# Performance work log

Hardware: AMD Instinct MI355X
Metric: run time of the kernel (lower is better)

## Reference

```python
import jax, jax.numpy as jnp
import numpy as np
from jax import lax

NUM_CLASSES = 80
CONF_THRE = 0.01   # testconf in source
NMS_THRE = 0.2     # nmsthresh in source
N = 8400           # YOLOX anchors at 640x640: 80^2+40^2+20^2
IMG = 640.0


def setup_inputs() -> dict:
    key = jax.random.key(0)
    pred = jax.random.uniform(key, (N, 5 + NUM_CLASSES), dtype=jnp.float32)
    # scale cx,cy,w,h to pixel units so boxes are realistic
    pred = pred.at[:, :4].multiply(IMG)
    return {"prediction": pred}


def _pairwise_iou(boxes):
    # boxes: [N,4] in x1,y1,x2,y2
    area = (boxes[:, 2] - boxes[:, 0]) * (boxes[:, 3] - boxes[:, 1])  # [N]
    lt = jnp.maximum(boxes[:, None, :2], boxes[None, :, :2])  # [N,N,2]
    rb = jnp.minimum(boxes[:, None, 2:], boxes[None, :, 2:])  # [N,N,2]
    wh = jnp.clip(rb - lt, 0.0)
    inter = wh[..., 0] * wh[..., 1]
    return inter / (area[:, None] + area[None, :] - inter + 1e-9)


def reference(prediction):
    # ---- box corner decode (cx,cy,w,h -> x1,y1,x2,y2) ----
    cx, cy, w, h = prediction[:, 0], prediction[:, 1], prediction[:, 2], prediction[:, 3]
    boxes = jnp.stack([cx - w / 2, cy - h / 2, cx + w / 2, cy + h / 2], axis=1)

    # ---- per-class max ----
    cls_scores = prediction[:, 5:5 + NUM_CLASSES]
    class_conf = jnp.max(cls_scores, axis=1, keepdims=True)            # [N,1]
    class_pred = jnp.argmax(cls_scores, axis=1).astype(prediction.dtype)[:, None]

    obj = prediction[:, 4]
    valid = obj >= CONF_THRE                                            # conf mask

    # detections = [x1,y1,x2,y2, obj_conf, class_conf, class_pred]  -> [N,7]
    det = jnp.concatenate([boxes, obj[:, None], class_conf, class_pred], axis=1)

    # ---- class-agnostic greedy NMS on obj score (fixed-shape version) ----
    scores = jnp.where(valid, obj, -1.0)
    order = jnp.argsort(-scores)
    det_s = det[order]
    boxes_s = boxes[order]
    valid_s = valid[order]

    iou = _pairwise_iou(boxes_s)  # [N,N] ~282MB, dominant traffic
    idx = jnp.arange(N)

    def step(keep, inp):
        i, row, v = inp
        alive = keep[i] & v                      # only a kept valid box suppresses
        supp = alive & (row > NMS_THRE) & (idx > i)
        return keep & ~supp, None

    keep0 = jnp.ones((N,), dtype=bool)
    keep, _ = lax.scan(step, keep0, (idx, iou, valid_s))
    keep = keep & valid_s

    # suppressed / below-conf rows are zeroed (torch returns a ragged subset;
    # here we return the score-sorted, mask-zeroed fixed-shape equivalent)
    out = det_s * keep[:, None].astype(det_s.dtype)
    return out
```

## Files before the change

kernel.cpp:

```cpp
#include <hip/hip_runtime.h>
#include <stdint.h>

#define N_BOX 8400
#define NCLS 80
#define PSTRIDE 85
#define NW 132
#define NTILE 8778
#define ZROWI N_BOX
#define CONF_T 0.01f
#define NMS_T 0.2f

typedef unsigned long long u64;

#define OFF_DET     0
#define OFF_DIAGT   0
#define OFF_SUP1    67584
#define OFF_SUP2    135168
#define OFF_KEYS    268800
#define OFF_DETS    336000
#define OFF_BOXESS  604800
#define OFF_MASK    739200
#define OFF_KEEPW   9610656
#define OFF_VCNT    9611712

__device__ __forceinline__ unsigned fmap_desc(float f) {
    unsigned u = __float_as_uint(f);
    unsigned m = (u & 0x80000000u) ? ~u : (u | 0x80000000u);
    return ~m;
}

__device__ __forceinline__ u64 readlane64(u64 v, int lane) {
    unsigned lo = (unsigned)__builtin_amdgcn_readlane((int)(unsigned)v, lane);
    unsigned hi = (unsigned)__builtin_amdgcn_readlane((int)(unsigned)(v >> 32), lane);
    return ((u64)hi << 32) | lo;
}

__device__ __forceinline__ u64 shfl_xor64(u64 v, int m) {
    int lo = __shfl_xor((int)(unsigned)v, m);
    int hi = __shfl_xor((int)(unsigned)(v >> 32), m);
    return ((u64)(unsigned)hi << 32) | (unsigned)lo;
}

__device__ __forceinline__ u64 bittranspose64(u64 x, int lane) {
    const u64 P0 = 0x5555555555555555ull, P1 = 0x3333333333333333ull,
              P2 = 0x0F0F0F0F0F0F0F0Full, P3 = 0x00FF00FF00FF00FFull,
              P4 = 0x0000FFFF0000FFFFull, P5 = 0x00000000FFFFFFFFull;
#define TSTEP(s, p) do {                                                 \
        u64 y = shfl_xor64(x, s);                                        \
        x = (lane & (s)) ? ((x & ~(p)) | ((y & ~(p)) >> (s)))            \
                         : ((x & (p))  | ((y & (p))  << (s)));           \
    } while (0)
    TSTEP(1, P0); TSTEP(2, P1); TSTEP(4, P2);
    TSTEP(8, P3); TSTEP(16, P4); TSTEP(32, P5);
#undef TSTEP
    return x;
}

__device__ __forceinline__ u64 wmask(int w, int V) {
    int nb = V - (w << 6);
    if (nb <= 0) return 0ull;
    if (nb >= 64) return ~0ull;
    return (1ull << nb) - 1ull;
}

__global__ __launch_bounds__(256) void prep_k(const float* __restrict__ pred,
                                              float* __restrict__ det,
                                              u64* __restrict__ keys,
                                              u64* __restrict__ mask) {
    if (blockIdx.x == 0 && threadIdx.x < NW)
        mask[(size_t)ZROWI * NW + threadIdx.x] = 0ull;
    int gt = blockIdx.x * 256 + threadIdx.x;
    int i = gt >> 2, q = gt & 3;
    if (i >= N_BOX) return;
    const float* p = pred + (size_t)i * PSTRIDE;
    int cbase = q * 20;
    float best = p[5 + cbase];
    int arg = cbase;
    for (int c = 1; c < 20; ++c) {
        float v = p[5 + cbase + c];
        if (v > best) { best = v; arg = cbase + c; }
    }
    for (int d = 1; d < 4; d <<= 1) {
        float ob = __shfl_xor(best, d);
        int   oa = __shfl_xor(arg, d);
        if (ob > best || (ob == best && oa < arg)) { best = ob; arg = oa; }
    }
    if (q == 0) {
        float cx = p[0], cy = p[1], w = p[2], h = p[3], obj = p[4];
        float hw = __fmul_rn(w, 0.5f), hh = __fmul_rn(h, 0.5f);
        float x1 = __fsub_rn(cx, hw), y1 = __fsub_rn(cy, hh);
        float x2 = __fadd_rn(cx, hw), y2 = __fadd_rn(cy, hh);
        bool valid = (obj >= CONF_T);
        float score = valid ? obj : -1.0f;
        keys[i] = ((u64)fmap_desc(score) << 32) | (unsigned)i;
        float4* dr = (float4*)(det + (size_t)i * 8);
        dr[0] = make_float4(x1, y1, x2, y2);
        dr[1] = make_float4(obj, best, (float)arg, 0.0f);
    }
}

__global__ __launch_bounds__(256) void rank_k(const u64* __restrict__ keys,
                                              const float* __restrict__ det,
                                              float4* __restrict__ det_s,
                                              float4* __restrict__ boxes_s,
                                              int* __restrict__ vcount) {
    int t = threadIdx.x;
    int i = blockIdx.x * 32 + (t & 31);
    int s = t >> 5;
    u64 my = (i < N_BOX) ? keys[i] : ~0ull;
    int cnt = 0, cv = 0;
    int j0 = s * 1050, j1 = j0 + 1050;
    for (int j = j0; j < j1; j += 2) {
        ulonglong2 kk = *(const ulonglong2*)(keys + j);
        cnt += (kk.x < my) + (kk.y < my);
        cv  += ((long long)kk.x >= 0) + ((long long)kk.y >= 0);
    }
    __shared__ int sc[256], sv[256];
    sc[t] = cnt; sv[t] = cv;
    __syncthreads();
    if (t < 32) {
        int r = sc[t] + sc[t + 32] + sc[t + 64] + sc[t + 96]
              + sc[t + 128] + sc[t + 160] + sc[t + 192] + sc[t + 224];
        if (i < N_BOX) {
            const float4* dr = (const float4*)(det + (size_t)i * 8);
            float4 b0 = dr[0], b1 = dr[1];
            det_s[(size_t)r * 2]     = b0;
            det_s[(size_t)r * 2 + 1] = b1;
            boxes_s[r] = b0;
        }
        if (blockIdx.x == 0 && t == 0) {
            *vcount = sv[0] + sv[32] + sv[64] + sv[96]
                    + sv[128] + sv[160] + sv[192] + sv[224];
        }
    }
}

__global__ __launch_bounds__(64) void mask_k(const float4* __restrict__ boxes_s,
                                             u64* __restrict__ mask,
                                             u64* __restrict__ diagT,
                                             u64* __restrict__ sup1,
                                             u64* __restrict__ sup2) {
    int tt = blockIdx.x, lane = threadIdx.x;
    int rb = (int)((2.0f * NW + 1.0f
                    - sqrtf((2.0f * NW + 1.0f) * (2.0f * NW + 1.0f) - 8.0f * (float)tt)) * 0.5f);
    while (rb > 0 && rb * NW - rb * (rb - 1) / 2 > tt) rb--;
    while ((rb + 1) * NW - (rb + 1) * rb / 2 <= tt) rb++;
    int cb = rb + (tt - (rb * NW - rb * (rb - 1) / 2));

    __shared__ float4 cB[64];
    __shared__ float  cA[64];
    int c0 = cb * 64 + lane;
    float4 b = (c0 < N_BOX) ? boxes_s[c0] : make_float4(0.f, 0.f, 0.f, 0.f);
    cB[lane] = b;
    cA[lane] = __fmul_rn(__fsub_rn(b.z, b.x), __fsub_rn(b.w, b.y));
    __syncthreads();
    int r = rb * 64 + lane;
    bool inb = (r < N_BOX);
    float4 rx = boxes_s[inb ? r : (N_BOX - 1)];
    float ra = __fmul_rn(__fsub_rn(rx.z, rx.x), __fsub_rn(rx.w, rx.y));
    u64 bits = 0ull;
    int cbase = cb * 64;
    for (int j = 0; j < 64; ++j) {
        int c = cbase + j;
        if (c >= N_BOX || c <= r) continue;
        float4 cx4 = cB[j];
        float ltx = fmaxf(rx.x, cx4.x), lty = fmaxf(rx.y, cx4.y);
        float rbx = fminf(rx.z, cx4.z), rby = fminf(rx.w, cx4.w);
        float wx = fmaxf(__fsub_rn(rbx, ltx), 0.0f);
        float wy = fmaxf(__fsub_rn(rby, lty), 0.0f);
        float inter = __fmul_rn(wx, wy);
        float denom = __fadd_rn(__fsub_rn(__fadd_rn(ra, cA[j]), inter), 1e-9f);
        float iou = __fdiv_rn(inter, denom);
        if (iou > NMS_T) bits |= (1ull << j);
    }
    if (inb) mask[(size_t)r * NW + cb] = bits;
    int d = cb - rb;
    if (d <= 2) {
        u64 tb = bittranspose64(bits, lane);
        size_t idx = (size_t)cb * 64 + lane;
        if (d == 0)      diagT[idx] = tb;
        else if (d == 1) sup1[idx]  = tb;
        else             sup2[idx]  = tb;
    }
}

__global__ __launch_bounds__(64, 1) void scan_k(const u64* __restrict__ mask,
                                                const u64* __restrict__ diagT,
                                                const u64* __restrict__ sup1,
                                                const u64* __restrict__ sup2,
                                                const int* __restrict__ vcount,
                                                u64* __restrict__ keepw) {
    int lane = threadIdx.x;
    int V = *vcount;
    int tw = (lane < 4) ? (128 + lane) : 131;
    u64 Ra = 0ull, Rb = 0ull, Rc = 0ull;
    u64 A1 = 0ull, A2 = 0ull;

#define DECLS(P) u64 P##A0=0,P##A1=0,P##A2=0,P##A3=0,P##A4=0,P##A5=0,P##A6=0,P##A7=0, \
                     P##B0=0,P##B1=0,P##B2=0,P##B3=0,P##B4=0,P##B5=0,P##B6=0,P##B7=0, \
                     P##C0=0,P##C1=0,P##C2=0,P##C3=0,P##C4=0,P##C5=0,P##C6=0,P##C7=0
    DECLS(s0); DECLS(s1); DECLS(s2);
#undef DECLS
    u64 td0,t10,t20, td1,t11,t21, td2,t12,t22, td3,t13,t23, td4,t14,t24, td5,t15,t25;

#define TLOAD(TD, T1, T2, wtv) do {                                      \
        int wt_ = (wtv); wt_ = wt_ < NW ? wt_ : (NW - 1);                \
        size_t ix_ = (size_t)wt_ * 64 + lane;                            \
        TD = diagT[ix_]; T1 = sup1[ix_]; T2 = sup2[ix_];                 \
    } while (0)

#define CONSUME(P) do {                                                  \
        Ra |= ((P##A0|P##A1)|(P##A2|P##A3))|((P##A4|P##A5)|(P##A6|P##A7));\
        Rb |= ((P##B0|P##B1)|(P##B2|P##B3))|((P##B4|P##B5)|(P##B6|P##B7));\
        Rc |= ((P##C0|P##C1)|(P##C2|P##C3))|((P##C4|P##C5)|(P##C6|P##C7));\
    } while (0)

#define ISSUE(P, i) do {                                                 \
        size_t ri_ = rem_ ? (size_t)(rb_ + __builtin_ctzll(rem_))        \
                          : (size_t)ZROWI;                               \
        rem_ &= rem_ - 1;                                                \
        const u64* rp_ = mask + ri_ * NW;                                \
        ulonglong2 v_ = *(const ulonglong2*)(rp_ + 2 * lane);            \
        P##A##i = v_.x; P##B##i = v_.y; P##C##i = rp_[tw];               \
    } while (0)

#define STEP(wv, P, TDu, T1u, T2u, TDl, T1l, T2l) do {                   \
        int w_ = (wv);                                                   \
        CONSUME(P);                          \
        TLOAD(TDl, T1l, T2l, w_ + 2);               \
        u64 rw_ = (w_ < 128) ? ((w_ & 1) ? Rb : Ra) : Rc;                \
        int sl_ = (w_ < 128) ? (w_ >> 1) : (w_ - 128);                   \
        u64 cur_ = readlane64(rw_, sl_);                                 \
        cur_ |= __ballot((T1u & A1) != 0ull);                            \
        cur_ |= __ballot((T2u & A2) != 0ull);                            \
        u64 m_ = wmask(w_, V);                                           \
        u64 ns_ = (~cur_) & m_;                                          \
        u64 L_ = 0ull;                                                   \
        while (ns_) {                           \
            int b_ = __builtin_ctzll(ns_);                               \
            L_ |= 1ull << b_;                                            \
            u64 sup_ = __ballot((int)((TDu >> b_) & 1ull));              \
            ns_ &= ~sup_;                                                \
            ns_ &= ~(1ull << b_);                                        \
        }                                                                \
        if (lane == 0) keepw[w_] = L_;                                   \
        A2 = A1; A1 = L_;                                                \
        u64 rem_ = L_; int rb_ = w_ << 6;                                \
        ISSUE(P, 0); ISSUE(P, 1); ISSUE(P, 2); ISSUE(P, 3);              \
        ISSUE(P, 4); ISSUE(P, 5); ISSUE(P, 6); ISSUE(P, 7);              \
        while (rem_) {                             \
            u64 xa_ = 0, xb_ = 0, xc_ = 0;                               \
            for (int q_ = 0; q_ < 4; ++q_) {                             \
                size_t ri_ = rem_ ? (size_t)(rb_ + __builtin_ctzll(rem_))\
                                  : (size_t)ZROWI;                       \
                rem_ &= rem_ - 1;                                        \
                const u64* rp_ = mask + ri_ * NW;                        \
                ulonglong2 v_ = *(const ulonglong2*)(rp_ + 2 * lane);    \
                xa_ |= v_.x; xb_ |= v_.y; xc_ |= rp_[tw];                \
            }                                                            \
            Ra |= xa_; Rb |= xb_; Rc |= xc_;                             \
        }                                                                \
    } while (0)

    TLOAD(td0, t10, t20, 0);
    TLOAD(td1, t11, t21, 1);

    for (int c = 0; c < NW; c += 6) {
        STEP(c + 0, s0, td0, t10, t20, td2, t12, t22);
        STEP(c + 1, s1, td1, t11, t21, td3, t13, t23);
        STEP(c + 2, s2, td2, t12, t22, td4, t14, t24);
        STEP(c + 3, s0, td3, t13, t23, td5, t15, t25);
        STEP(c + 4, s1, td4, t14, t24, td0, t10, t20);
        STEP(c + 5, s2, td5, t15, t25, td1, t11, t21);
    }
#undef STEP
#undef ISSUE
#undef CONSUME
#undef TLOAD
}

__global__ __launch_bounds__(256) void out_k(const float* __restrict__ det_s,
                                             const u64* __restrict__ keepw,
                                             float* __restrict__ out) {
    int e = blockIdx.x * 256 + threadIdx.x;
    if (e >= N_BOX * 7) return;
    int r = e / 7, c = e - r * 7;
    bool k = (keepw[r >> 6] >> (r & 63)) & 1ull;
    out[e] = k ? det_s[r * 8 + c] : 0.0f;
}

extern "C" void kernel_launch(void* const* d_in, const int* in_sizes, int n_in,
                              void* d_out, int out_size, void* d_ws, size_t ws_size,
                              hipStream_t stream) {
    const float* pred = (const float*)d_in[0];
    char* ws = (char*)d_ws;
    float*  det     = (float*) (ws + OFF_DET);
    u64*    diagT   = (u64*)   (ws + OFF_DIAGT);
    u64*    sup1    = (u64*)   (ws + OFF_SUP1);
    u64*    sup2    = (u64*)   (ws + OFF_SUP2);
    u64*    keys    = (u64*)   (ws + OFF_KEYS);
    float*  det_s   = (float*) (ws + OFF_DETS);
    float4* boxes_s = (float4*)(ws + OFF_BOXESS);
    u64*    mask    = (u64*)   (ws + OFF_MASK);
    u64*    keepw   = (u64*)   (ws + OFF_KEEPW);
    int*    vcount  = (int*)   (ws + OFF_VCNT);

    prep_k<<<132, 256, 0, stream>>>(pred, det, keys, mask);
    rank_k<<<264, 256, 0, stream>>>(keys, det, (float4*)det_s, boxes_s, vcount);
    mask_k<<<NTILE, 64, 0, stream>>>(boxes_s, mask, diagT, sup1, sup2);
    scan_k<<<1, 64, 0, stream>>>(mask, diagT, sup1, sup2, vcount, keepw);
    out_k <<<(N_BOX * 7 + 255) / 256, 256, 0, stream>>>(det_s, keepw, (float*)d_out);
}
```

Baseline: 156.3 us.

## Split NMS scan into decision and row-OR waves synchronized via LDS barriers

```diff
diff --git a/kernel.cpp b/kernel.cpp
--- a/kernel.cpp
+++ b/kernel.cpp
@@ -16,6 +16,7 @@
 #define OFF_DIAGT   0
 #define OFF_SUP1    67584
 #define OFF_SUP2    135168
+#define OFF_SUP3    202752
 #define OFF_KEYS    268800
 #define OFF_DETS    336000
 #define OFF_BOXESS  604800
@@ -61,6 +62,12 @@
     if (nb <= 0) return 0ull;
     if (nb >= 64) return ~0ull;
     return (1ull << nb) - 1ull;
+}
+
+__device__ __forceinline__ void step_barrier() {
+    asm volatile("s_waitcnt lgkmcnt(0)" ::: "memory");
+    __builtin_amdgcn_s_barrier();
+    asm volatile("" ::: "memory");
 }
 
 __global__ __launch_bounds__(256) void prep_k(const float* __restrict__ pred,
@@ -139,7 +146,8 @@
                                              u64* __restrict__ mask,
                                              u64* __restrict__ diagT,
                                              u64* __restrict__ sup1,
-                                             u64* __restrict__ sup2) {
+                                             u64* __restrict__ sup2,
+                                             u64* __restrict__ sup3) {
     int tt = blockIdx.x, lane = threadIdx.x;
     int rb = (int)((2.0f * NW + 1.0f
                     - sqrtf((2.0f * NW + 1.0f) * (2.0f * NW + 1.0f) - 8.0f * (float)tt)) * 0.5f);
@@ -175,108 +183,133 @@
     }
     if (inb) mask[(size_t)r * NW + cb] = bits;
     int d = cb - rb;
-    if (d <= 2) {
+    if (d <= 3) {
         u64 tb = bittranspose64(bits, lane);
         size_t idx = (size_t)cb * 64 + lane;
         if (d == 0)      diagT[idx] = tb;
         else if (d == 1) sup1[idx]  = tb;
-        else             sup2[idx]  = tb;
-    }
-}
-
-__global__ __launch_bounds__(64, 1) void scan_k(const u64* __restrict__ mask,
-                                                const u64* __restrict__ diagT,
-                                                const u64* __restrict__ sup1,
-                                                const u64* __restrict__ sup2,
-                                                const int* __restrict__ vcount,
-                                                u64* __restrict__ keepw) {
-    int lane = threadIdx.x;
+        else if (d == 2) sup2[idx]  = tb;
+        else             sup3[idx]  = tb;
+    }
+}
+
+__global__ __launch_bounds__(128, 1) void scan_k(const u64* __restrict__ mask,
+                                                 const u64* __restrict__ diagT,
+                                                 const u64* __restrict__ sup1,
+                                                 const u64* __restrict__ sup2,
+                                                 const u64* __restrict__ sup3,
+                                                 const int* __restrict__ vcount,
+                                                 u64* __restrict__ keepw) {
+    __shared__ u64 remvP[NW + 2];
+    __shared__ u64 Lbuf[NW];
+    int tid = threadIdx.x, lane = tid & 63, wv = tid >> 6;
     int V = *vcount;
-    int tw = (lane < 4) ? (128 + lane) : 131;
-    u64 Ra = 0ull, Rb = 0ull, Rc = 0ull;
-    u64 A1 = 0ull, A2 = 0ull;
-
-#define DECLS(P) u64 P##A0=0,P##A1=0,P##A2=0,P##A3=0,P##A4=0,P##A5=0,P##A6=0,P##A7=0, \
-                     P##B0=0,P##B1=0,P##B2=0,P##B3=0,P##B4=0,P##B5=0,P##B6=0,P##B7=0, \
-                     P##C0=0,P##C1=0,P##C2=0,P##C3=0,P##C4=0,P##C5=0,P##C6=0,P##C7=0
-    DECLS(s0); DECLS(s1); DECLS(s2);
-#undef DECLS
-    u64 td0,t10,t20, td1,t11,t21, td2,t12,t22, td3,t13,t23, td4,t14,t24, td5,t15,t25;
-
-#define TLOAD(TD, T1, T2, wtv) do {                                      \
-        int wt_ = (wtv); wt_ = wt_ < NW ? wt_ : (NW - 1);                \
-        size_t ix_ = (size_t)wt_ * 64 + lane;                            \
-        TD = diagT[ix_]; T1 = sup1[ix_]; T2 = sup2[ix_];                 \
-    } while (0)
-
-#define CONSUME(P) do {                                                  \
-        Ra |= ((P##A0|P##A1)|(P##A2|P##A3))|((P##A4|P##A5)|(P##A6|P##A7));\
-        Rb |= ((P##B0|P##B1)|(P##B2|P##B3))|((P##B4|P##B5)|(P##B6|P##B7));\
-        Rc |= ((P##C0|P##C1)|(P##C2|P##C3))|((P##C4|P##C5)|(P##C6|P##C7));\
-    } while (0)
-
-#define ISSUE(P, i) do {                                                 \
-        size_t ri_ = rem_ ? (size_t)(rb_ + __builtin_ctzll(rem_))        \
-                          : (size_t)ZROWI;                               \
-        rem_ &= rem_ - 1;                                                \
-        const u64* rp_ = mask + ri_ * NW;                                \
-        ulonglong2 v_ = *(const ulonglong2*)(rp_ + 2 * lane);            \
-        P##A##i = v_.x; P##B##i = v_.y; P##C##i = rp_[tw];               \
-    } while (0)
-
-#define STEP(wv, P, TDu, T1u, T2u, TDl, T1l, T2l) do {                   \
-        int w_ = (wv);                                                   \
-        CONSUME(P);                          \
-        TLOAD(TDl, T1l, T2l, w_ + 2);               \
-        u64 rw_ = (w_ < 128) ? ((w_ & 1) ? Rb : Ra) : Rc;                \
-        int sl_ = (w_ < 128) ? (w_ >> 1) : (w_ - 128);                   \
-        u64 cur_ = readlane64(rw_, sl_);                                 \
-        cur_ |= __ballot((T1u & A1) != 0ull);                            \
-        cur_ |= __ballot((T2u & A2) != 0ull);                            \
-        u64 m_ = wmask(w_, V);                                           \
+    for (int i = tid; i < NW + 2; i += 128) remvP[i] = 0ull;
+    __syncthreads();
+
+    if (wv == 0) {
+        u64 A1 = 0ull, A2 = 0ull, A3 = 0ull;
+        u64 d0P, s1P, s2P, s3P, d0Q, s1Q, s2Q, s3Q;
+
+#define TL(S, kk) do {                                                   \
+        int t_ = (kk) < NW ? (kk) : (NW - 1);                            \
+        size_t ix_ = (size_t)t_ * 64 + lane;                             \
+        d0##S = diagT[ix_]; s1##S = sup1[ix_];                           \
+        s2##S = sup2[ix_];  s3##S = sup3[ix_];                           \
+    } while (0)
+
+#define STEP0(kk, S) do {                                                \
+        int k_ = (kk);                                                   \
+        u64 cur_ = remvP[k_];                                            \
+        cur_ |= __ballot((s1##S & A1) != 0ull);                          \
+        cur_ |= __ballot((s2##S & A2) != 0ull);                          \
+        cur_ |= __ballot((s3##S & A3) != 0ull);                          \
+        u64 m_ = wmask(k_, V);                                           \
         u64 ns_ = (~cur_) & m_;                                          \
         u64 L_ = 0ull;                                                   \
-        while (ns_) {                           \
+        while (ns_) {                                                    \
             int b_ = __builtin_ctzll(ns_);                               \
             L_ |= 1ull << b_;                                            \
-            u64 sup_ = __ballot((int)((TDu >> b_) & 1ull));              \
+            u64 sup_ = __ballot((int)((d0##S >> b_) & 1ull));            \
             ns_ &= ~sup_;                                                \
             ns_ &= ~(1ull << b_);                                        \
         }                                                                \
-        if (lane == 0) keepw[w_] = L_;                                   \
-        A2 = A1; A1 = L_;                                                \
-        u64 rem_ = L_; int rb_ = w_ << 6;                                \
-        ISSUE(P, 0); ISSUE(P, 1); ISSUE(P, 2); ISSUE(P, 3);              \
-        ISSUE(P, 4); ISSUE(P, 5); ISSUE(P, 6); ISSUE(P, 7);              \
+        if (lane == 0) { Lbuf[k_] = L_; keepw[k_] = L_; }                \
+        A3 = A2; A2 = A1; A1 = L_;                                       \
+        TL(S, k_ + 2);                                                   \
+        step_barrier();                                                  \
+    } while (0)
+
+        TL(P, 0);
+        TL(Q, 1);
+        for (int c = 0; c < NW; c += 2) {
+            STEP0(c + 0, P);
+            STEP0(c + 1, Q);
+        }
+#undef STEP0
+#undef TL
+    } else {
+        int tw = (lane < 4) ? (128 + lane) : 131;
+        u64 Ra = 0ull, Rb = 0ull, Rc = 0ull;
+        u64 Pa0=0,Pa1=0,Pa2=0,Pa3=0,Pa4=0,Pa5=0,Pa6=0,Pa7=0;
+        u64 Pb0=0,Pb1=0,Pb2=0,Pb3=0,Pb4=0,Pb5=0,Pb6=0,Pb7=0;
+        u64 Pc0=0,Pc1=0,Pc2=0,Pc3=0,Pc4=0,Pc5=0,Pc6=0,Pc7=0;
+        u64 Qa0=0,Qa1=0,Qa2=0,Qa3=0,Qa4=0,Qa5=0,Qa6=0,Qa7=0;
+        u64 Qb0=0,Qb1=0,Qb2=0,Qb3=0,Qb4=0,Qb5=0,Qb6=0,Qb7=0;
+        u64 Qc0=0,Qc1=0,Qc2=0,Qc3=0,Qc4=0,Qc5=0,Qc6=0,Qc7=0;
+
+#define CONS(S) do {                                                     \
+        Ra |= ((S##a0|S##a1)|(S##a2|S##a3))|((S##a4|S##a5)|(S##a6|S##a7));\
+        Rb |= ((S##b0|S##b1)|(S##b2|S##b3))|((S##b4|S##b5)|(S##b6|S##b7));\
+        Rc |= ((S##c0|S##c1)|(S##c2|S##c3))|((S##c4|S##c5)|(S##c6|S##c7));\
+    } while (0)
+
+#define LROW(S, i) do {                                                  \
+        size_t ri_ = rem_ ? (size_t)(rbase_ + __builtin_ctzll(rem_))     \
+                          : (size_t)ZROWI;                               \
+        rem_ &= rem_ - 1ull;                                             \
+        const u64* rp_ = mask + ri_ * NW;                                \
+        ulonglong2 v_ = *(const ulonglong2*)(rp_ + 2 * lane);            \
+        S##a##i = v_.x; S##b##i = v_.y; S##c##i = rp_[tw];               \
+    } while (0)
+
+#define STEP1(jj, S) do {                                                \
+        int j_ = (jj);                                                   \
+        CONS(S);                                  \
+        int w_ = j_ + 1;                                                 \
+        u64 rw_ = (w_ < 128) ? ((w_ & 1) ? Rb : Ra) : Rc;                \
+        int sl_ = (w_ < 128) ? (w_ >> 1) : (w_ - 128);                   \
+        u64 pv_ = readlane64(rw_, sl_);                                  \
+        if (lane == 0) remvP[w_] = pv_;                                  \
+        u64 Lp_ = Lbuf[j_ >= 1 ? j_ - 1 : 0];                            \
+        if (j_ < 1) Lp_ = 0ull;                                          \
+        int rbase_ = (j_ - 1) << 6;                                      \
+        u64 rem_ = Lp_;                                                  \
+        LROW(S, 0); LROW(S, 1); LROW(S, 2); LROW(S, 3);                  \
+        LROW(S, 4); LROW(S, 5); LROW(S, 6); LROW(S, 7);                  \
         while (rem_) {                             \
             u64 xa_ = 0, xb_ = 0, xc_ = 0;                               \
-            for (int q_ = 0; q_ < 4; ++q_) {                             \
-                size_t ri_ = rem_ ? (size_t)(rb_ + __builtin_ctzll(rem_))\
+            for (int q_ = 0; q_ < 16; ++q_) {                            \
+                size_t ri_ = rem_ ? (size_t)(rbase_ + __builtin_ctzll(rem_)) \
                                   : (size_t)ZROWI;                       \
-                rem_ &= rem_ - 1;                                        \
+                rem_ &= rem_ - 1ull;                                     \
                 const u64* rp_ = mask + ri_ * NW;                        \
                 ulonglong2 v_ = *(const ulonglong2*)(rp_ + 2 * lane);    \
                 xa_ |= v_.x; xb_ |= v_.y; xc_ |= rp_[tw];                \
             }                                                            \
             Ra |= xa_; Rb |= xb_; Rc |= xc_;                             \
         }                                                                \
-    } while (0)
-
-    TLOAD(td0, t10, t20, 0);
-    TLOAD(td1, t11, t21, 1);
-
-    for (int c = 0; c < NW; c += 6) {
-        STEP(c + 0, s0, td0, t10, t20, td2, t12, t22);
-        STEP(c + 1, s1, td1, t11, t21, td3, t13, t23);
-        STEP(c + 2, s2, td2, t12, t22, td4, t14, t24);
-        STEP(c + 3, s0, td3, t13, t23, td5, t15, t25);
-        STEP(c + 4, s1, td4, t14, t24, td0, t10, t20);
-        STEP(c + 5, s2, td5, t15, t25, td1, t11, t21);
-    }
-#undef STEP
-#undef ISSUE
-#undef CONSUME
-#undef TLOAD
+        step_barrier();                                                  \
+    } while (0)
+
+        for (int c = 0; c < NW; c += 2) {
+            STEP1(c + 0, P);
+            STEP1(c + 1, Q);
+        }
+#undef STEP1
+#undef LROW
+#undef CONS
+    }
 }
 
 __global__ __launch_bounds__(256) void out_k(const float* __restrict__ det_s,
@@ -298,6 +331,7 @@
     u64*    diagT   = (u64*)   (ws + OFF_DIAGT);
     u64*    sup1    = (u64*)   (ws + OFF_SUP1);
     u64*    sup2    = (u64*)   (ws + OFF_SUP2);
+    u64*    sup3    = (u64*)   (ws + OFF_SUP3);
     u64*    keys    = (u64*)   (ws + OFF_KEYS);
     float*  det_s   = (float*) (ws + OFF_DETS);
     float4* boxes_s = (float4*)(ws + OFF_BOXESS);
@@ -307,7 +341,7 @@
 
     prep_k<<<132, 256, 0, stream>>>(pred, det, keys, mask);
     rank_k<<<264, 256, 0, stream>>>(keys, det, (float4*)det_s, boxes_s, vcount);
-    mask_k<<<NTILE, 64, 0, stream>>>(boxes_s, mask, diagT, sup1, sup2);
-    scan_k<<<1, 64, 0, stream>>>(mask, diagT, sup1, sup2, vcount, keepw);
+    mask_k<<<NTILE, 64, 0, stream>>>(boxes_s, mask, diagT, sup1, sup2, sup3);
+    scan_k<<<1, 128, 0, stream>>>(mask, diagT, sup1, sup2, sup3, vcount, keepw);
     out_k <<<(N_BOX * 7 + 255) / 256, 256, 0, stream>>>(det_s, keepw, (float*)d_out);
 }
```

Measured after the change: 153.8 us. No clear change (-1.6%).
